# Kernel optimization log

Measured on AMD Instinct MI355X. Metric: run time of the kernel, lower is better.

## Reference

```python
import jax, jax.numpy as jnp
from jax import lax
import numpy as np

N, K, QK, W = 10, 10, 150, 128
D = 256
HID = 100
CHANS = [1, 16, 32, 64, 128, 256]
STRIDES = [2, 2, 1, 1, 1]
ITERS = 3
BN_EPS = 1e-5


def setup_inputs() -> dict:
    key = jax.random.key(0)
    ks = jax.random.split(key, 12)
    inp = {
        "support": jax.random.normal(ks[0], (N, K, 1, W, W), jnp.float32),
        "query": jax.random.normal(ks[1], (QK, 1, W, W), jnp.float32),
    }
    for i in range(5):
        inp[f"conv_w{i}"] = jax.random.normal(ks[2 + i], (CHANS[i + 1], CHANS[i], 3, 3), jnp.float32) * 0.05
        inp[f"bn_g{i}"] = jnp.ones((CHANS[i + 1],), jnp.float32)
        inp[f"bn_b{i}"] = jnp.zeros((CHANS[i + 1],), jnp.float32)
    inp["trans_w"] = jax.random.normal(ks[8], (D, D), jnp.float32) * 0.05
    inp["trans_b"] = jnp.zeros((D,), jnp.float32)
    inp["bil_w"] = jax.random.normal(ks[9], (HID, D, D), jnp.float32) * 0.02
    inp["score_w"] = jax.random.normal(ks[10], (1, HID), jnp.float32) * 0.1
    inp["score_b"] = jnp.zeros((1,), jnp.float32)
    return inp


def _block(x, w, g, b, s):
    # Conv2d(k=3, pad=1, stride=s, no bias) -> BatchNorm(eval: mean=0, var=1) -> ReLU -> MaxPool2d(2)
    x = lax.conv_general_dilated(x, w, (s, s), ((1, 1), (1, 1)),
                                 dimension_numbers=('NCHW', 'OIHW', 'NCHW'))
    scale = (g / jnp.sqrt(1.0 + BN_EPS))[None, :, None, None]
    x = jax.nn.relu(x * scale + b[None, :, None, None])
    return lax.reduce_window(x, -jnp.inf, lax.max, (1, 1, 2, 2), (1, 1, 2, 2), 'VALID')


def reference(support, query,
              conv_w0, conv_w1, conv_w2, conv_w3, conv_w4,
              bn_g0, bn_g1, bn_g2, bn_g3, bn_g4,
              bn_b0, bn_b1, bn_b2, bn_b3, bn_b4,
              trans_w, trans_b, bil_w, score_w, score_b):
    n, k = support.shape[0], support.shape[1]
    qk = query.shape[0]
    w = support.shape[3]

    ws = [conv_w0, conv_w1, conv_w2, conv_w3, conv_w4]
    gs = [bn_g0, bn_g1, bn_g2, bn_g3, bn_g4]
    bs = [bn_b0, bn_b1, bn_b2, bn_b3, bn_b4]

    # run the conv backbone on support+query jointly (BN is per-sample in eval mode)
    x = jnp.concatenate([support.reshape(n * k, 1, w, w), query], axis=0)
    for cw, g, b, s in zip(ws, gs, bs, STRIDES):
        x = _block(x, cw, g, b, s)
    feats = x.reshape(x.shape[0], -1)              # (n*k + qk, 256); spatial is 1x1
    sup = feats[:n * k].reshape(n, k, -1)          # (n, k, d)
    q = feats[n * k:]                              # (qk, d)

    # dynamic routing: Transformer(e) is recomputed each iter on the same input -> hoist
    e = sup @ trans_w.T + trans_b                  # (n, k, d)
    b0 = jnp.zeros((n, k), sup.dtype)

    def step(bb, _):
        dcoef = jax.nn.softmax(bb, axis=1)[:, :, None]   # (n, k, 1)
        c = (dcoef * e).sum(axis=1)                      # (n, d)
        cn = jnp.sqrt((c * c).sum(axis=1, keepdims=True))
        c = c * (cn / (cn * cn + 1.0))                   # squash: ||c||^2/(||c||^2+1)/||c||
        db = (c[:, None, :] * e).sum(axis=2)             # (n, k)
        return bb + db, c

    _, cs = lax.scan(step, b0, None, length=ITERS)
    proto = cs[-1]                                  # (n, d)

    # NTN: bilinear score for every (query, proto) pair, exploiting the pair structure
    t1 = jnp.einsum('nc,hce->nhe', proto, bil_w)    # (n, HID, d)
    v = jnp.einsum('nhe,qe->qnh', t1, q)            # (qk, n, HID)
    s = jax.nn.relu(v) @ score_w[0] + score_b[0]    # (qk, n)
    return jax.nn.log_softmax(s, axis=1)
```

## Files before the change

### kernel.cpp

```cpp
#include <hip/hip_runtime.h>
#include <math.h>


#define BN_SCALE rsqrtf(1.0f + 1e-5f)

#define OFF_FEATS 0
#define OFF_E     64000
#define OFF_S     89600
#define OFF_T1    91136
#define OFF_PROTO 347136
#define OFF_W1T   349696
#define OFF_W2T   354304
#define OFF_W3T   372736
#define OFF_W4T   446464
#define OFF_TWT   741376

__global__ void k_prep(const float* __restrict__ w1, const float* __restrict__ w2,
                       const float* __restrict__ w3, const float* __restrict__ w4,
                       const float* __restrict__ tw, float* __restrict__ ws) {
  float* w1t = ws + OFF_W1T;
  float* w2t = ws + OFF_W2T;
  float* w3t = ws + OFF_W3T;
  float* w4t = ws + OFF_W4T;
  float* twt = ws + OFF_TWT;
  int i = blockIdx.x * 256 + threadIdx.x;
  if (i < 4608) {
    int oc = i & 31; int r = i >> 5; int tap = r % 9; int ic = r / 9;
    w1t[i] = w1[(oc * 16 + ic) * 9 + tap];
  } else if (i < 23040) {
    int j = i - 4608;
    int oc = j & 63; int r = j >> 6; int tap = r % 9; int ic = r / 9;
    w2t[j] = w2[(oc * 32 + ic) * 9 + tap];
  } else if (i < 96768) {
    int j = i - 23040;
    int oc = j & 127; int r = j >> 7; int tap = r % 9; int ic = r / 9;
    w3t[j] = w3[(oc * 64 + ic) * 9 + tap];
  } else if (i < 391680) {
    int j = i - 96768;
    int oc = j & 255; int r = j >> 8; int tap = r % 9; int ic = r / 9;
    w4t[j] = w4[(oc * 128 + ic) * 9 + tap];
  } else if (i < 457216) {
    int j = i - 391680;
    int d = j >> 8, c = j & 255;
    twt[j] = tw[c * 256 + d];
  } else if (i < 713216) {
    ws[OFF_T1 + (i - 457216)] = 0.f;
  } else if (i < 714716) {
    ws[OFF_S + (i - 713216)] = 0.f;
  }
}

__global__ void __launch_bounds__(1024, 4)
k_main(const float* __restrict__ sup, const float* __restrict__ qry,
       const float* __restrict__ w0, const float* __restrict__ g0, const float* __restrict__ b0,
       const float* __restrict__ g1, const float* __restrict__ b1,
       const float* __restrict__ g2, const float* __restrict__ b2,
       const float* __restrict__ g3, const float* __restrict__ b3,
       const float* __restrict__ g4, const float* __restrict__ b4,
       const float* __restrict__ tb, float* __restrict__ ws,
       float* __restrict__ feats_g, float* __restrict__ e_buf) {
  __shared__ float S[28164];
  const float* w1t = ws + OFF_W1T;
  const float* w2t = ws + OFF_W2T;
  const float* w3t = ws + OFF_W3T;
  const float* w4t = ws + OFF_W4T;
  const float* twt = ws + OFF_TWT;
  const int img = blockIdx.x;
  const int t = threadIdx.x;
  const int lane = t & 63, wid = t >> 6;
  float* a0p = S + 8580;
  float* sa1 = S;
  float* sa2 = S + 4096;
  float* sa3 = S + 7424;
  float* sft = S + 7936;
  float* RED = S + 8580;

  const float* in = (img < 100) ? (sup + (size_t)img * 16384)
                                : (qry + (size_t)(img - 100) * 16384);

  {
    int oc = wid;
    float wv[9];
#pragma unroll
    for (int k = 0; k < 9; k++) wv[k] = w0[oc * 9 + k];
    float sc = g0[oc] * BN_SCALE, bs = b0[oc];
    int pcol = lane & 31, prh = lane >> 5;

    for (int i = t; i < 19584; i += 1024) a0p[i] = 0.f;

    for (int pass = 0; pass < 2; pass++) {
      __syncthreads();
      for (int i = t; i < 8580; i += 1024) {
        int r = i / 132, c = i % 132;
        int ir = pass ? (63 + r) : (r - 1);
        int icl = c - 1;
        S[i] = (ir >= 0 && ir < 128 && icl >= 0 && icl < 128) ? in[ir * 128 + icl] : 0.f;
      }
      __syncthreads();
#pragma unroll
      for (int it = 0; it < 8; it++) {
        int prl = it * 2 + prh;
        float win[25];
#pragma unroll
        for (int d = 0; d < 5; d++) {
          const float* rp = S + (4 * prl + d) * 132 + 4 * pcol;
          float4 r4 = *(const float4*)rp;
          win[d * 5 + 0] = r4.x; win[d * 5 + 1] = r4.y;
          win[d * 5 + 2] = r4.z; win[d * 5 + 3] = r4.w;
          win[d * 5 + 4] = rp[4];
        }
        float m = -1e30f;
#pragma unroll
        for (int a = 0; a < 2; a++)
#pragma unroll
          for (int b = 0; b < 2; b++) {
            float c = 0.f;
#pragma unroll
            for (int ky = 0; ky < 3; ky++)
#pragma unroll
              for (int kx = 0; kx < 3; kx++)
                c = fmaf(win[(2 * a + ky) * 5 + (2 * b + kx)], wv[ky * 3 + kx], c);
            m = fmaxf(m, fmaf(c, sc, bs));
          }
        int PR = pass * 16 + prl;
        a0p[oc * 1224 + (PR + 1) * 36 + (pcol + 1)] = fmaxf(m, 0.f);
      }
    }
  }
  __syncthreads();
  for (int i = t; i < 7424; i += 1024) S[i] = 0.f;
  __syncthreads();

  {
    int ocp = t & 15, pos = t >> 4;
    int py = pos >> 3, px = pos & 7;
    float acc0[4] = {0.f, 0.f, 0.f, 0.f}, acc1[4] = {0.f, 0.f, 0.f, 0.f};
    float2 wc[9];
#pragma unroll
    for (int k = 0; k < 9; k++) wc[k] = *(const float2*)(w1t + k * 32 + 2 * ocp);
    for (int ic = 0; ic < 16; ic++) {
      float2 wn[9];
      if (ic < 15) {
#pragma unroll
        for (int k = 0; k < 9; k++)
          wn[k] = *(const float2*)(w1t + ((ic + 1) * 9 + k) * 32 + 2 * ocp);
      }
      float win[25];
      const float* bp = a0p + ic * 1224 + 4 * py * 36 + 4 * px;
#pragma unroll
      for (int d = 0; d < 5; d++) {
        float4 r4 = *(const float4*)(bp + d * 36);
        win[d * 5 + 0] = r4.x; win[d * 5 + 1] = r4.y;
        win[d * 5 + 2] = r4.z; win[d * 5 + 3] = r4.w;
        win[d * 5 + 4] = bp[d * 36 + 4];
      }
#pragma unroll
      for (int cy = 0; cy < 2; cy++)
#pragma unroll
        for (int cx = 0; cx < 2; cx++) {
          float c0 = acc0[cy * 2 + cx], c1 = acc1[cy * 2 + cx];
#pragma unroll
          for (int ky = 0; ky < 3; ky++)
#pragma unroll
            for (int kx = 0; kx < 3; kx++) {
              float iv = win[(2 * cy + ky) * 5 + (2 * cx + kx)];
              c0 = fmaf(iv, wc[ky * 3 + kx].x, c0);
              c1 = fmaf(iv, wc[ky * 3 + kx].y, c1);
            }
          acc0[cy * 2 + cx] = c0; acc1[cy * 2 + cx] = c1;
        }
      if (ic < 15) {
#pragma unroll
        for (int k = 0; k < 9; k++) wc[k] = wn[k];
      }
    }
#pragma unroll
    for (int j = 0; j < 2; j++) {
      int oc = 2 * ocp + j;
      const float* ac = j ? acc1 : acc0;
      float sc = g1[oc] * BN_SCALE, bsj = b1[oc];
      float m = -1e30f;
#pragma unroll
      for (int p = 0; p < 4; p++) m = fmaxf(m, fmaf(ac[p], sc, bsj));
      sa1[oc * 124 + (py + 1) * 12 + (px + 1)] = fmaxf(m, 0.f);
    }
  }
  __syncthreads();

  {
    int oc = t & 63, icg = (t >> 6) & 3, pg = t >> 8;
    int pgy = pg >> 1, pgx = pg & 1;
    float acc[16];
#pragma unroll
    for (int p = 0; p < 16; p++) acc[p] = 0.f;
    float wc[9];
    {
      const float* wp = w2t + (icg * 8) * 576 + oc;
#pragma unroll
      for (int k = 0; k < 9; k++) wc[k] = wp[k * 64];
    }
    for (int ii = 0; ii < 8; ii++) {
      int ic = icg * 8 + ii;
      float wn[9];
      if (ii < 7) {
        const float* wp = w2t + (ic + 1) * 576 + oc;
#pragma unroll
        for (int k = 0; k < 9; k++) wn[k] = wp[k * 64];
      }
      float win[6][6];
      const float* bp = sa1 + ic * 124 + 4 * pgy * 12 + 4 * pgx;
#pragma unroll
      for (int d = 0; d < 6; d++) {
        float4 u = *(const float4*)(bp + d * 12);
        float2 v = *(const float2*)(bp + d * 12 + 4);
        win[d][0] = u.x; win[d][1] = u.y; win[d][2] = u.z; win[d][3] = u.w;
        win[d][4] = v.x; win[d][5] = v.y;
      }
#pragma unroll
      for (int u = 0; u < 4; u++)
#pragma unroll
        for (int v = 0; v < 4; v++) {
          float c = acc[u * 4 + v];
#pragma unroll
          for (int ky = 0; ky < 3; ky++)
#pragma unroll
            for (int kx = 0; kx < 3; kx++)
              c = fmaf(win[u + ky][v + kx], wc[ky * 3 + kx], c);
          acc[u * 4 + v] = c;
        }
      if (ii < 7) {
#pragma unroll
        for (int k = 0; k < 9; k++) wc[k] = wn[k];
      }
    }
#pragma unroll
    for (int j = 0; j < 16; j++) RED[j * 1024 + icg * 256 + pg * 64 + oc] = acc[j];
  }
  __syncthreads();
  if (t < 256) {
    int oc = t & 63, pg = t >> 6;
    int pgy = pg >> 1, pgx = pg & 1;
    float sc = g2[oc] * BN_SCALE, bsj = b2[oc];
#pragma unroll
    for (int cy = 0; cy < 2; cy++)
#pragma unroll
      for (int cx = 0; cx < 2; cx++) {
        float m = -1e30f;
#pragma unroll
        for (int a = 0; a < 2; a++)
#pragma unroll
          for (int b = 0; b < 2; b++) {
            int j = (2 * cy + a) * 4 + (2 * cx + b);
            float v = RED[j * 1024 + pg * 64 + oc] + RED[j * 1024 + 256 + pg * 64 + oc]
                    + RED[j * 1024 + 512 + pg * 64 + oc] + RED[j * 1024 + 768 + pg * 64 + oc];
            m = fmaxf(m, fmaf(v, sc, bsj));
          }
        sa2[oc * 52 + (1 + 2 * pgy + cy) * 8 + (1 + 2 * pgx + cx)] = fmaxf(m, 0.f);
      }
  }
  __syncthreads();

  {
    int oc = t & 127, icg = t >> 7;
    float acc[16];
#pragma unroll
    for (int p = 0; p < 16; p++) acc[p] = 0.f;
    float wc[9];
    {
      const float* wp = w3t + (icg * 8) * 1152 + oc;
#pragma unroll
      for (int k = 0; k < 9; k++) wc[k] = wp[k * 128];
    }
    for (int ii = 0; ii < 8; ii++) {
      int ic = icg * 8 + ii;
      float wn[9];
      if (ii < 7) {
        const float* wp = w3t + (ic + 1) * 1152 + oc;
#pragma unroll
        for (int k = 0; k < 9; k++) wn[k] = wp[k * 128];
      }
      float win[6][6];
      const float* bp = sa2 + ic * 52;
#pragma unroll
      for (int d = 0; d < 6; d++) {
        float4 u = *(const float4*)(bp + d * 8);
        float2 v = *(const float2*)(bp + d * 8 + 4);
        win[d][0] = u.x; win[d][1] = u.y; win[d][2] = u.z; win[d][3] = u.w;
        win[d][4] = v.x; win[d][5] = v.y;
      }
#pragma unroll
      for (int u = 0; u < 4; u++)
#pragma unroll
        for (int v = 0; v < 4; v++) {
          float c = acc[u * 4 + v];
#pragma unroll
          for (int ky = 0; ky < 3; ky++)
#pragma unroll
            for (int kx = 0; kx < 3; kx++)
              c = fmaf(win[u + ky][v + kx], wc[ky * 3 + kx], c);
          acc[u * 4 + v] = c;
        }
      if (ii < 7) {
#pragma unroll
        for (int k = 0; k < 9; k++) wc[k] = wn[k];
      }
    }
#pragma unroll
    for (int j = 0; j < 16; j++) RED[j * 1024 + icg * 128 + oc] = acc[j];
  }
  __syncthreads();
  if (t < 512) {
    int oc = t & 127, pp = t >> 7;
    int py = pp >> 1, px = pp & 1;
    float sc = g3[oc] * BN_SCALE, bsj = b3[oc];
    float m = -1e30f;
#pragma unroll
    for (int a = 0; a < 2; a++)
#pragma unroll
      for (int b = 0; b < 2; b++) {
        int j = (2 * py + a) * 4 + (2 * px + b);
        float v = 0.f;
#pragma unroll
        for (int g = 0; g < 8; g++) v += RED[j * 1024 + g * 128 + oc];
        m = fmaxf(m, fmaf(v, sc, bsj));
      }
    sa3[oc * 4 + pp] = fmaxf(m, 0.f);
  }
  __syncthreads();

  {
    int oc = t & 255, icq = t >> 8;
    float acc[4] = {0.f, 0.f, 0.f, 0.f};
    float wc[9];
    {
      const float* wp = w4t + (icq * 32) * 2304 + oc;
#pragma unroll
      for (int k = 0; k < 9; k++) wc[k] = wp[k * 256];
    }
    for (int ii = 0; ii < 32; ii++) {
      int ic = icq * 32 + ii;
      float wn[9];
      if (ii < 31) {
        const float* wp = w4t + (ic + 1) * 2304 + oc;
#pragma unroll
        for (int k = 0; k < 9; k++) wn[k] = wp[k * 256];
      }
      float4 iv = *(const float4*)(sa3 + ic * 4);
#pragma unroll
      for (int py = 0; py < 2; py++)
#pragma unroll
        for (int px = 0; px < 2; px++) {
          float c = acc[py * 2 + px];
          c = fmaf(iv.x, wc[(1 - py) * 3 + (1 - px)], c);
          c = fmaf(iv.y, wc[(1 - py) * 3 + (2 - px)], c);
          c = fmaf(iv.z, wc[(2 - py) * 3 + (1 - px)], c);
          c = fmaf(iv.w, wc[(2 - py) * 3 + (2 - px)], c);
          acc[py * 2 + px] = c;
        }
      if (ii < 31) {
#pragma unroll
        for (int k = 0; k < 9; k++) wc[k] = wn[k];
      }
    }
    if (icq) {
#pragma unroll
      for (int p = 0; p < 4; p++) RED[((icq - 1) * 256 + oc) * 4 + p] = acc[p];
    }
    __syncthreads();
    if (icq == 0) {
      float sc = g4[oc] * BN_SCALE, bsj = b4[oc];
      float m = -1e30f;
#pragma unroll
      for (int p = 0; p < 4; p++) {
        float v = acc[p] + RED[oc * 4 + p] + RED[(256 + oc) * 4 + p] + RED[(512 + oc) * 4 + p];
        m = fmaxf(m, fmaf(v, sc, bsj));
      }
      float r = fmaxf(m, 0.f);
      sft[oc] = r;
      feats_g[(size_t)img * 256 + oc] = r;
    }
  }
  __syncthreads();

  if (img < 100) {
    int c = t & 255, dq = t >> 8;
    float acc = 0.f;
    float wv = twt[(dq * 64) * 256 + c];
#pragma unroll 4
    for (int ii = 0; ii < 64; ii++) {
      int d = dq * 64 + ii;
      float wnext = (ii < 63) ? twt[(d + 1) * 256 + c] : 0.f;
      acc = fmaf(sft[d], wv, acc);
      wv = wnext;
    }
    if (dq) RED[(dq - 1) * 256 + c] = acc;
    __syncthreads();
    if (dq == 0)
      e_buf[img * 256 + c] = acc + RED[c] + RED[256 + c] + RED[512 + c] + tb[c];
  }
}

__global__ void k_routing(const float* __restrict__ e, float* __restrict__ proto) {
  int n = blockIdx.x;
  __shared__ float sb[10], sdc[10], red[4], red2[40], sfc[1];
  int t = threadIdx.x;
  int lane = t & 63, wid = t >> 6;
  float ek[10];
#pragma unroll
  for (int k = 0; k < 10; k++) ek[k] = e[n * 2560 + k * 256 + t];
  if (t < 10) sb[t] = 0.f;
  __syncthreads();
  float cd = 0.f;
  for (int iter = 0; iter < 3; iter++) {
    if (t == 0) {
      float mx = sb[0];
      for (int k = 1; k < 10; k++) mx = fmaxf(mx, sb[k]);
      float sum = 0.f;
      for (int k = 0; k < 10; k++) { float ex = expf(sb[k] - mx); sdc[k] = ex; sum += ex; }
      float inv = 1.f / sum;
      for (int k = 0; k < 10; k++) sdc[k] *= inv;
    }
    __syncthreads();
    cd = 0.f;
#pragma unroll
    for (int k = 0; k < 10; k++) cd = fmaf(sdc[k], ek[k], cd);
    float ss = cd * cd;
#pragma unroll
    for (int off = 32; off > 0; off >>= 1) ss += __shfl_down(ss, off, 64);
    if (lane == 0) red[wid] = ss;
    __syncthreads();
    if (t == 0) {
      float tot = red[0] + red[1] + red[2] + red[3];
      sfc[0] = sqrtf(tot) / (tot + 1.f);
    }
    __syncthreads();
    cd *= sfc[0];
    float pr[10];
#pragma unroll
    for (int k = 0; k < 10; k++) pr[k] = cd * ek[k];
#pragma unroll
    for (int off = 32; off > 0; off >>= 1)
#pragma unroll
      for (int k = 0; k < 10; k++) pr[k] += __shfl_down(pr[k], off, 64);
    if (lane == 0)
#pragma unroll
      for (int k = 0; k < 10; k++) red2[k * 4 + wid] = pr[k];
    __syncthreads();
    if (t < 10) sb[t] += red2[t * 4] + red2[t * 4 + 1] + red2[t * 4 + 2] + red2[t * 4 + 3];
    __syncthreads();
  }
  proto[n * 256 + t] = cd;
}

__global__ void k_t1(const float* __restrict__ proto, const float* __restrict__ bw,
                     float* __restrict__ t1) {
  __shared__ float pt[384];
  const int b = blockIdx.x;
  const int h = b >> 3, c0 = (b & 7) * 32;
  const int t = threadIdx.x;
  for (int i = t; i < 320; i += 256) {
    int n = i >> 5, cl = i & 31;
    pt[cl * 12 + n] = proto[n * 256 + c0 + cl];
  }
  __syncthreads();
  float acc[10];
#pragma unroll
  for (int n = 0; n < 10; n++) acc[n] = 0.f;
  const float* wp = bw + (size_t)h * 65536 + (size_t)c0 * 256 + t;
#pragma unroll 4
  for (int cl = 0; cl < 32; cl++) {
    float wv = wp[(size_t)cl * 256];
    float4 p0 = *(const float4*)(pt + cl * 12);
    float4 p1 = *(const float4*)(pt + cl * 12 + 4);
    float2 p2 = *(const float2*)(pt + cl * 12 + 8);
    acc[0] = fmaf(p0.x, wv, acc[0]); acc[1] = fmaf(p0.y, wv, acc[1]);
    acc[2] = fmaf(p0.z, wv, acc[2]); acc[3] = fmaf(p0.w, wv, acc[3]);
    acc[4] = fmaf(p1.x, wv, acc[4]); acc[5] = fmaf(p1.y, wv, acc[5]);
    acc[6] = fmaf(p1.z, wv, acc[6]); acc[7] = fmaf(p1.w, wv, acc[7]);
    acc[8] = fmaf(p2.x, wv, acc[8]); acc[9] = fmaf(p2.y, wv, acc[9]);
  }
#pragma unroll
  for (int n = 0; n < 10; n++)
    atomicAdd(&t1[((size_t)n * 100 + h) * 256 + t], acc[n]);
}

__global__ void k_score(const float* __restrict__ t1, const float* __restrict__ qf,
                        const float* __restrict__ sw, float* __restrict__ s) {
  __shared__ float sq[256];
  __shared__ float vb[2000];
  const int q = blockIdx.x >> 1, hh = blockIdx.x & 1;
  const int t = threadIdx.x;
  const int sl = t & 3, quad = t >> 2;
  sq[t] = qf[q * 256 + t];
  __syncthreads();
  const float4* qr = (const float4*)sq;
#pragma unroll
  for (int j = 0; j < 8; j++) {
    int lr = quad + 64 * j;
    if (lr < 500) {
      int n = lr / 50, hl = lr % 50;
      const float4* row = (const float4*)(t1 + ((size_t)(n * 100 + hh * 50 + hl)) * 256);
      float acc = 0.f;
#pragma unroll
      for (int d = 0; d < 16; d++) {
        float4 a = row[d * 4 + sl];
        float4 b = qr[d * 4 + sl];
        acc += a.x * b.x + a.y * b.y + a.z * b.z + a.w * b.w;
      }
      vb[lr * 4 + sl] = acc;
    }
  }
  __syncthreads();
  if (t < 10) {
    float sum = 0.f;
    for (int hl = 0; hl < 50; hl++) {
      int lr = t * 50 + hl;
      float d = vb[lr * 4] + vb[lr * 4 + 1] + vb[lr * 4 + 2] + vb[lr * 4 + 3];
      sum = fmaf(fmaxf(d, 0.f), sw[hh * 50 + hl], sum);
    }
    atomicAdd(&s[q * 10 + t], sum);
  }
}

__global__ void k_lsm(const float* __restrict__ s, const float* __restrict__ sbp,
                      float* __restrict__ out) {
  int q = threadIdx.x;
  if (q >= 150) return;
  float sb0 = sbp[0];
  float v[10];
  float mx = -1e30f;
#pragma unroll
  for (int n = 0; n < 10; n++) {
    v[n] = s[q * 10 + n] + sb0;
    mx = fmaxf(mx, v[n]);
  }
  float sum = 0.f;
#pragma unroll
  for (int n = 0; n < 10; n++) sum += expf(v[n] - mx);
  float lse = mx + logf(sum);
#pragma unroll
  for (int n = 0; n < 10; n++) out[q * 10 + n] = v[n] - lse;
}

extern "C" void kernel_launch(void* const* d_in, const int* in_sizes, int n_in,
                              void* d_out, int out_size, void* d_ws, size_t ws_size,
                              hipStream_t stream) {
  const float* support = (const float*)d_in[0];
  const float* query   = (const float*)d_in[1];
  const float* conv_w[5]; const float* bn_g[5]; const float* bn_b[5];
  for (int i = 0; i < 5; i++) {
    conv_w[i] = (const float*)d_in[2 + 3 * i];
    bn_g[i]   = (const float*)d_in[3 + 3 * i];
    bn_b[i]   = (const float*)d_in[4 + 3 * i];
  }
  const float* trans_w = (const float*)d_in[17];
  const float* trans_b = (const float*)d_in[18];
  const float* bil_w   = (const float*)d_in[19];
  const float* score_w = (const float*)d_in[20];
  const float* score_b = (const float*)d_in[21];
  float* out = (float*)d_out;
  float* ws = (float*)d_ws;

  float* feats = ws + OFF_FEATS;
  float* e_buf = ws + OFF_E;
  float* s_buf = ws + OFF_S;
  float* t1    = ws + OFF_T1;
  float* proto = ws + OFF_PROTO;

  k_prep<<<2793, 256, 0, stream>>>(conv_w[1], conv_w[2], conv_w[3], conv_w[4],
                                   trans_w, ws);
  k_main<<<250, 1024, 0, stream>>>(support, query,
                                   conv_w[0], bn_g[0], bn_b[0],
                                   bn_g[1], bn_b[1], bn_g[2], bn_b[2],
                                   bn_g[3], bn_b[3], bn_g[4], bn_b[4],
                                   trans_b, ws, feats, e_buf);
  k_routing<<<10, 256, 0, stream>>>(e_buf, proto);
  k_t1<<<800, 256, 0, stream>>>(proto, bil_w, t1);
  k_score<<<300, 256, 0, stream>>>(t1, feats + 100 * 256, score_w, s_buf);
  k_lsm<<<1, 256, 0, stream>>>(s_buf, score_b, out);
}
```

Baseline: 212.8 us.

## Restructure first two conv layers and fuse log-softmax into score kernel

Layer 0 now reads the input image directly from global memory with a row-based register stencil instead of staging two halves through shared memory. Layer 1 splits input channels across two thread groups, gives each thread 4 output channels, and combines the partial sums through a new shared reduction buffer. The final log-softmax kernel is removed and run by the last-finishing score block, detected with an atomic counter, which saves one launch. The t1 loop unroll also grows from 4 to 8. The larger shared array may lower occupancy, and the counter adds atomic and fence overhead.

```diff
diff --git a/kernel.cpp b/kernel.cpp
--- a/kernel.cpp
+++ b/kernel.cpp
@@ -14,6 +14,7 @@
 #define OFF_W3T   372736
 #define OFF_W4T   446464
 #define OFF_TWT   741376
+#define OFF_CNT   (OFF_S + 1500)
 
 __global__ void k_prep(const float* __restrict__ w1, const float* __restrict__ w2,
                        const float* __restrict__ w3, const float* __restrict__ w4,
@@ -45,7 +46,7 @@
     twt[j] = tw[c * 256 + d];
   } else if (i < 713216) {
     ws[OFF_T1 + (i - 457216)] = 0.f;
-  } else if (i < 714716) {
+  } else if (i < 714717) {
     ws[OFF_S + (i - 713216)] = 0.f;
   }
 }
@@ -59,7 +60,7 @@
        const float* __restrict__ g4, const float* __restrict__ b4,
        const float* __restrict__ tb, float* __restrict__ ws,
        float* __restrict__ feats_g, float* __restrict__ e_buf) {
-  __shared__ float S[28164];
+  __shared__ float S[38404];
   const float* w1t = ws + OFF_W1T;
   const float* w2t = ws + OFF_W2T;
   const float* w3t = ws + OFF_W3T;
@@ -68,83 +69,97 @@
   const int img = blockIdx.x;
   const int t = threadIdx.x;
   const int lane = t & 63, wid = t >> 6;
-  float* a0p = S + 8580;
   float* sa1 = S;
   float* sa2 = S + 4096;
   float* sa3 = S + 7424;
   float* sft = S + 7936;
+  float* a0p = S + 8580;
   float* RED = S + 8580;
+  float* L1R = S + 28164;
 
   const float* in = (img < 100) ? (sup + (size_t)img * 16384)
                                 : (qry + (size_t)(img - 100) * 16384);
 
+  for (int i = t; i < 7424; i += 1024) S[i] = 0.f;
+  for (int i = t; i < 19584; i += 1024) a0p[i] = 0.f;
+  __syncthreads();
+
   {
-    int oc = wid;
+    const int oc = wid;
     float wv[9];
 #pragma unroll
     for (int k = 0; k < 9; k++) wv[k] = w0[oc * 9 + k];
-    float sc = g0[oc] * BN_SCALE, bs = b0[oc];
-    int pcol = lane & 31, prh = lane >> 5;
-
-    for (int i = t; i < 19584; i += 1024) a0p[i] = 0.f;
-
-    for (int pass = 0; pass < 2; pass++) {
-      __syncthreads();
-      for (int i = t; i < 8580; i += 1024) {
-        int r = i / 132, c = i % 132;
-        int ir = pass ? (63 + r) : (r - 1);
-        int icl = c - 1;
-        S[i] = (ir >= 0 && ir < 128 && icl >= 0 && icl < 128) ? in[ir * 128 + icl] : 0.f;
-      }
-      __syncthreads();
-#pragma unroll
-      for (int it = 0; it < 8; it++) {
-        int prl = it * 2 + prh;
-        float win[25];
-#pragma unroll
-        for (int d = 0; d < 5; d++) {
-          const float* rp = S + (4 * prl + d) * 132 + 4 * pcol;
-          float4 r4 = *(const float4*)rp;
-          win[d * 5 + 0] = r4.x; win[d * 5 + 1] = r4.y;
-          win[d * 5 + 2] = r4.z; win[d * 5 + 3] = r4.w;
-          win[d * 5 + 4] = rp[4];
+    const float sc = g0[oc] * BN_SCALE, bs = b0[oc];
+#pragma unroll 2
+    for (int it2 = 0; it2 < 4; it2++) {
+      const int s2 = it2 * 64 + lane;
+      const int pr = s2 >> 3, pcq = s2 & 7;
+      float acc[2][8];
+#pragma unroll
+      for (int j = 0; j < 8; j++) { acc[0][j] = 0.f; acc[1][j] = 0.f; }
+#pragma unroll
+      for (int d = 0; d < 5; d++) {
+        const int ir = 4 * pr - 1 + d;
+        float x[17];
+        if (ir >= 0) {
+          const float* rp = in + ir * 128 + 16 * pcq;
+          float4 q0 = ((const float4*)rp)[0];
+          float4 q1 = ((const float4*)rp)[1];
+          float4 q2 = ((const float4*)rp)[2];
+          float4 q3 = ((const float4*)rp)[3];
+          x[0] = (pcq > 0) ? rp[-1] : 0.f;
+          x[1] = q0.x;  x[2] = q0.y;  x[3] = q0.z;  x[4] = q0.w;
+          x[5] = q1.x;  x[6] = q1.y;  x[7] = q1.z;  x[8] = q1.w;
+          x[9] = q2.x;  x[10] = q2.y; x[11] = q2.z; x[12] = q2.w;
+          x[13] = q3.x; x[14] = q3.y; x[15] = q3.z; x[16] = q3.w;
+        } else {
+#pragma unroll
+          for (int k = 0; k < 17; k++) x[k] = 0.f;
         }
-        float m = -1e30f;
-#pragma unroll
-        for (int a = 0; a < 2; a++)
-#pragma unroll
-          for (int b = 0; b < 2; b++) {
-            float c = 0.f;
-#pragma unroll
-            for (int ky = 0; ky < 3; ky++)
-#pragma unroll
-              for (int kx = 0; kx < 3; kx++)
-                c = fmaf(win[(2 * a + ky) * 5 + (2 * b + kx)], wv[ky * 3 + kx], c);
-            m = fmaxf(m, fmaf(c, sc, bs));
-          }
-        int PR = pass * 16 + prl;
-        a0p[oc * 1224 + (PR + 1) * 36 + (pcol + 1)] = fmaxf(m, 0.f);
-      }
-    }
-  }
-  __syncthreads();
-  for (int i = t; i < 7424; i += 1024) S[i] = 0.f;
+        if (d <= 2) {
+          const int b9 = d * 3;
+#pragma unroll
+          for (int j = 0; j < 8; j++)
+            acc[0][j] = fmaf(x[2 * j + 2], wv[b9 + 2],
+                        fmaf(x[2 * j + 1], wv[b9 + 1],
+                        fmaf(x[2 * j],     wv[b9],     acc[0][j])));
+        }
+        if (d >= 2) {
+          const int b9 = (d - 2) * 3;
+#pragma unroll
+          for (int j = 0; j < 8; j++)
+            acc[1][j] = fmaf(x[2 * j + 2], wv[b9 + 2],
+                        fmaf(x[2 * j + 1], wv[b9 + 1],
+                        fmaf(x[2 * j],     wv[b9],     acc[1][j])));
+        }
+      }
+      float* op = a0p + oc * 1224 + (pr + 1) * 36 + 4 * pcq + 1;
+#pragma unroll
+      for (int p = 0; p < 4; p++) {
+        float m = fmaf(acc[0][2 * p], sc, bs);
+        m = fmaxf(m, fmaf(acc[0][2 * p + 1], sc, bs));
+        m = fmaxf(m, fmaf(acc[1][2 * p], sc, bs));
+        m = fmaxf(m, fmaf(acc[1][2 * p + 1], sc, bs));
+        op[p] = fmaxf(m, 0.f);
+      }
+    }
+  }
   __syncthreads();
 
   {
-    int ocp = t & 15, pos = t >> 4;
-    int py = pos >> 3, px = pos & 7;
-    float acc0[4] = {0.f, 0.f, 0.f, 0.f}, acc1[4] = {0.f, 0.f, 0.f, 0.f};
-    float2 wc[9];
-#pragma unroll
-    for (int k = 0; k < 9; k++) wc[k] = *(const float2*)(w1t + k * 32 + 2 * ocp);
-    for (int ic = 0; ic < 16; ic++) {
-      float2 wn[9];
-      if (ic < 15) {
-#pragma unroll
-        for (int k = 0; k < 9; k++)
-          wn[k] = *(const float2*)(w1t + ((ic + 1) * 9 + k) * 32 + 2 * ocp);
-      }
+    const int pos = t & 63, py = pos >> 3, px = pos & 7;
+    const int ocg = (t >> 6) & 7, icg = t >> 9;
+    float acc[4][4];
+#pragma unroll
+    for (int j = 0; j < 4; j++)
+#pragma unroll
+      for (int p = 0; p < 4; p++) acc[j][p] = 0.f;
+    for (int ii = 0; ii < 8; ii++) {
+      const int ic = icg * 8 + ii;
+      float4 wq[9];
+#pragma unroll
+      for (int k = 0; k < 9; k++)
+        wq[k] = *(const float4*)(w1t + (ic * 9 + k) * 32 + 4 * ocg);
       float win[25];
       const float* bp = a0p + ic * 1224 + 4 * py * 36 + 4 * px;
 #pragma unroll
@@ -158,31 +173,41 @@
       for (int cy = 0; cy < 2; cy++)
 #pragma unroll
         for (int cx = 0; cx < 2; cx++) {
-          float c0 = acc0[cy * 2 + cx], c1 = acc1[cy * 2 + cx];
+          const int p = cy * 2 + cx;
 #pragma unroll
           for (int ky = 0; ky < 3; ky++)
 #pragma unroll
             for (int kx = 0; kx < 3; kx++) {
-              float iv = win[(2 * cy + ky) * 5 + (2 * cx + kx)];
-              c0 = fmaf(iv, wc[ky * 3 + kx].x, c0);
-              c1 = fmaf(iv, wc[ky * 3 + kx].y, c1);
+              const float iv = win[(2 * cy + ky) * 5 + (2 * cx + kx)];
+              const float4 wk = wq[ky * 3 + kx];
+              acc[0][p] = fmaf(iv, wk.x, acc[0][p]);
+              acc[1][p] = fmaf(iv, wk.y, acc[1][p]);
+              acc[2][p] = fmaf(iv, wk.z, acc[2][p]);
+              acc[3][p] = fmaf(iv, wk.w, acc[3][p]);
             }
-          acc0[cy * 2 + cx] = c0; acc1[cy * 2 + cx] = c1;
         }
-      if (ic < 15) {
-#pragma unroll
-        for (int k = 0; k < 9; k++) wc[k] = wn[k];
-      }
-    }
-#pragma unroll
-    for (int j = 0; j < 2; j++) {
-      int oc = 2 * ocp + j;
-      const float* ac = j ? acc1 : acc0;
-      float sc = g1[oc] * BN_SCALE, bsj = b1[oc];
-      float m = -1e30f;
-#pragma unroll
-      for (int p = 0; p < 4; p++) m = fmaxf(m, fmaf(ac[p], sc, bsj));
-      sa1[oc * 124 + (py + 1) * 12 + (px + 1)] = fmaxf(m, 0.f);
+    }
+    const int slot = pos * 8 + ocg;
+    if (icg == 1) {
+      float* wp2 = L1R + slot * 20;
+#pragma unroll
+      for (int j = 0; j < 4; j++)
+        *(float4*)(wp2 + j * 4) = make_float4(acc[j][0], acc[j][1], acc[j][2], acc[j][3]);
+    }
+    __syncthreads();
+    if (icg == 0) {
+      const float* rp2 = L1R + slot * 20;
+#pragma unroll
+      for (int j = 0; j < 4; j++) {
+        float4 o = *(const float4*)(rp2 + j * 4);
+        const int oc = ocg * 4 + j;
+        const float sc = g1[oc] * BN_SCALE, bsj = b1[oc];
+        float m = fmaf(acc[j][0] + o.x, sc, bsj);
+        m = fmaxf(m, fmaf(acc[j][1] + o.y, sc, bsj));
+        m = fmaxf(m, fmaf(acc[j][2] + o.z, sc, bsj));
+        m = fmaxf(m, fmaf(acc[j][3] + o.w, sc, bsj));
+        sa1[oc * 124 + (py + 1) * 12 + (px + 1)] = fmaxf(m, 0.f);
+      }
     }
   }
   __syncthreads();
@@ -467,7 +492,7 @@
 #pragma unroll
   for (int n = 0; n < 10; n++) acc[n] = 0.f;
   const float* wp = bw + (size_t)h * 65536 + (size_t)c0 * 256 + t;
-#pragma unroll 4
+#pragma unroll 8
   for (int cl = 0; cl < 32; cl++) {
     float wv = wp[(size_t)cl * 256];
     float4 p0 = *(const float4*)(pt + cl * 12);
@@ -485,9 +510,12 @@
 }
 
 __global__ void k_score(const float* __restrict__ t1, const float* __restrict__ qf,
-                        const float* __restrict__ sw, float* __restrict__ s) {
+                        const float* __restrict__ sw, const float* __restrict__ sbp,
+                        float* __restrict__ s, unsigned* __restrict__ cnt,
+                        float* __restrict__ out) {
   __shared__ float sq[256];
   __shared__ float vb[2000];
+  __shared__ int lastFlag;
   const int q = blockIdx.x >> 1, hh = blockIdx.x & 1;
   const int t = threadIdx.x;
   const int sl = t & 3, quad = t >> 2;
@@ -519,27 +547,30 @@
       sum = fmaf(fmaxf(d, 0.f), sw[hh * 50 + hl], sum);
     }
     atomicAdd(&s[q * 10 + t], sum);
-  }
-}
-
-__global__ void k_lsm(const float* __restrict__ s, const float* __restrict__ sbp,
-                      float* __restrict__ out) {
-  int q = threadIdx.x;
-  if (q >= 150) return;
-  float sb0 = sbp[0];
-  float v[10];
-  float mx = -1e30f;
-#pragma unroll
-  for (int n = 0; n < 10; n++) {
-    v[n] = s[q * 10 + n] + sb0;
-    mx = fmaxf(mx, v[n]);
-  }
-  float sum = 0.f;
-#pragma unroll
-  for (int n = 0; n < 10; n++) sum += expf(v[n] - mx);
-  float lse = mx + logf(sum);
-#pragma unroll
-  for (int n = 0; n < 10; n++) out[q * 10 + n] = v[n] - lse;
+    __threadfence();
+  }
+  __syncthreads();
+  if (t == 0) {
+    unsigned old = atomicAdd(cnt, 1u);
+    lastFlag = (old == 299u);
+  }
+  __syncthreads();
+  if (lastFlag && t < 150) {
+    float sb0 = sbp[0];
+    float v[10];
+    float mx = -1e30f;
+#pragma unroll
+    for (int n = 0; n < 10; n++) {
+      v[n] = atomicAdd(&s[t * 10 + n], 0.f) + sb0;
+      mx = fmaxf(mx, v[n]);
+    }
+    float sum2 = 0.f;
+#pragma unroll
+    for (int n = 0; n < 10; n++) sum2 += expf(v[n] - mx);
+    float lse = mx + logf(sum2);
+#pragma unroll
+    for (int n = 0; n < 10; n++) out[t * 10 + n] = v[n] - lse;
+  }
 }
 
 extern "C" void kernel_launch(void* const* d_in, const int* in_sizes, int n_in,
@@ -566,6 +597,7 @@
   float* s_buf = ws + OFF_S;
   float* t1    = ws + OFF_T1;
   float* proto = ws + OFF_PROTO;
+  unsigned* cnt = (unsigned*)(ws + OFF_CNT);
 
   k_prep<<<2793, 256, 0, stream>>>(conv_w[1], conv_w[2], conv_w[3], conv_w[4],
                                    trans_w, ws);
@@ -576,6 +608,6 @@
                                    trans_b, ws, feats, e_buf);
   k_routing<<<10, 256, 0, stream>>>(e_buf, proto);
   k_t1<<<800, 256, 0, stream>>>(proto, bil_w, t1);
-  k_score<<<300, 256, 0, stream>>>(t1, feats + 100 * 256, score_w, s_buf);
-  k_lsm<<<1, 256, 0, stream>>>(s_buf, score_b, out);
+  k_score<<<300, 256, 0, stream>>>(t1, feats + 100 * 256, score_w, score_b,
+                                   s_buf, cnt, out);
 }
```

Result: slower. 224.2 us (+5.3%).
